# Optimization experiments

Measured on AMD Instinct MI355X. Metric: run time of the kernel, lower is better.

Reference implementation:

```python
import jax, jax.numpy as jnp
import numpy as np

N = 40000          # nodes
E = 1280000        # edges (avg degree 32)
S = 64             # num_scalars
V = 16             # num_vectors
R = 32             # num_radial
CUTOFF = 10.0


def setup_inputs() -> dict:
    key = jax.random.key(0)
    ks = jax.random.split(key, 12)
    scalars = jax.random.normal(ks[0], (N, S), dtype=jnp.float32)
    vectors = jax.random.normal(ks[1], (N, V, 3), dtype=jnp.float32)
    edge_index = jax.random.randint(ks[2], (2, E), 0, N, dtype=jnp.int64)
    edge_vec = jax.random.normal(ks[3], (E, 3), dtype=jnp.float32)
    # radial_net: Linear(R,R) -> SiLU -> Linear(R, S + 2V)
    W1 = jax.random.normal(ks[4], (R, R), dtype=jnp.float32) * 0.1
    b1 = jnp.zeros((R,), dtype=jnp.float32)
    W2 = jax.random.normal(ks[5], (R, S + 2 * V), dtype=jnp.float32) * 0.1
    b2 = jnp.zeros((S + 2 * V,), dtype=jnp.float32)
    # attention: Linear(2S+R, S) -> SiLU -> Linear(S, 1)
    Wa1 = jax.random.normal(ks[6], (2 * S + R, S), dtype=jnp.float32) * 0.1
    ba1 = jnp.zeros((S,), dtype=jnp.float32)
    Wa2 = jax.random.normal(ks[7], (S, 1), dtype=jnp.float32) * 0.1
    ba2 = jnp.zeros((1,), dtype=jnp.float32)
    return dict(scalars=scalars, vectors=vectors, edge_vec=edge_vec,
                W1=W1, b1=b1, W2=W2, b2=b2,
                Wa1=Wa1, ba1=ba1, Wa2=Wa2, ba2=ba2,
                edge_index=edge_index)


def reference(scalars, vectors, edge_vec, W1, b1, W2, b2, Wa1, ba1, Wa2, ba2, edge_index):
    src = edge_index[0]  # j (source)
    dst = edge_index[1]  # i (target / aggregation index)

    d = jnp.linalg.norm(edge_vec, axis=-1)                 # [E]
    d_safe = jnp.clip(d[:, None], 1e-8, None)              # [E,1]

    # Bessel radial basis with cosine cutoff
    freqs = (jnp.arange(1, R + 1, dtype=jnp.float32) * np.pi / CUTOFF)
    bessel = jnp.sin(freqs * d[:, None]) / d_safe          # [E,R]
    cut = 0.5 * (jnp.cos(np.pi * d[:, None] / CUTOFF) + 1.0)
    cut = cut * (d[:, None] < CUTOFF).astype(jnp.float32)
    rbf = bessel * cut                                     # [E,R]

    # spherical harmonics (lmax=1); vector already normalized, sh = [1, y, z, x]
    unit = edge_vec / d_safe                               # [E,3]
    sh_weight = jnp.stack([unit[:, 1], unit[:, 2], unit[:, 0]], axis=-1)  # [E,3]

    # radial filter MLP
    filters = jax.nn.silu(rbf @ W1 + b1) @ W2 + b2         # [E, S+2V]
    scalar_filter = filters[:, :S]
    vector_filter = filters[:, S:S + V]
    vector_gate = filters[:, S + V:]

    s_i = scalars[dst]                                     # [E,S]
    s_j = scalars[src]                                     # [E,S]
    v_j = vectors[src]                                     # [E,V,3]

    scalar_message = s_j * scalar_filter                   # [E,S]
    vector_message = (v_j * vector_filter[:, :, None]
                      + vector_gate[:, :, None] * sh_weight[:, None, :])  # [E,V,3]

    att_in = jnp.concatenate([s_i, s_j, rbf], axis=-1)     # [E, 2S+R]
    att = jax.nn.sigmoid(jax.nn.silu(att_in @ Wa1 + ba1) @ Wa2 + ba2)  # [E,1]

    scalar_message = att * scalar_message
    vector_message = att[:, :, None] * vector_message

    scalar_aggr = jax.ops.segment_sum(scalar_message, dst, num_segments=N)
    vector_aggr = jax.ops.segment_sum(vector_message, dst, num_segments=N)

    return scalars + scalar_aggr, vectors + vector_aggr
```

## Files before the change

kernel.cpp:

```cpp
#include <hip/hip_runtime.h>

static constexpr int N_ = 40000;
static constexpr int E_ = 1280000;
static constexpr int NS = N_ * 64;
static constexpr int NV = N_ * 48;

typedef _Float16 half2_t __attribute__((ext_vector_type(2)));
typedef _Float16 half8_t __attribute__((ext_vector_type(8)));
typedef float float4_t __attribute__((ext_vector_type(4)));
typedef unsigned int uint;

__device__ __forceinline__ float silu_f(float x) { return __fdividef(x, 1.f + __expf(-x)); }
__device__ __forceinline__ int rfl(int x) { return __builtin_amdgcn_readfirstlane(x); }

static constexpr int PATT_BLOCKS = 512;
__global__ __launch_bounds__(256) void k_patt(
    const float* __restrict__ scalars, const float* __restrict__ Wa1,
    const float* __restrict__ ba1,
    _Float16* __restrict__ P1h, _Float16* __restrict__ P2h)
{
    int gw   = (blockIdx.x * 256 + threadIdx.x) >> 6;
    int lane = threadIdx.x & 63;
    float w[128];
#pragma unroll
    for (int k = 0; k < 128; k++) w[k] = Wa1[k * 64 + lane];
    float bias = ba1[lane];
    for (int n = gw; n < N_; n += PATT_BLOCKS * 4) {
        float sv = scalars[(size_t)n * 64 + lane];
        float a1 = bias, a2 = 0.f;
#pragma unroll
        for (int k = 0; k < 64; k++) {
            float sk = __shfl(sv, k, 64);
            a1 = fmaf(sk, w[k], a1);
            a2 = fmaf(sk, w[64 + k], a2);
        }
        P1h[(size_t)n * 64 + lane] = (_Float16)a1;
        P2h[(size_t)n * 64 + lane] = (_Float16)a2;
    }
}

__global__ void k_convp(const float* __restrict__ scalars, const float* __restrict__ vectors,
                        _Float16* __restrict__ sc16p, _Float16* __restrict__ vec16p,
                        const float* __restrict__ W1, const float* __restrict__ Wa1,
                        const float* __restrict__ W2, uint* __restrict__ tbl,
                        uint* __restrict__ tbl2)
{
    if (blockIdx.x >= 5000) {
        int t = (blockIdx.x - 5000) * 256 + threadIdx.x;
        if (t < 1536) {
            int j = t >> 4, q = t & 15;
            int k0 = 2 * q, k1 = 2 * q + 1;
            float a = (j < 64) ? Wa1[(128 + k0) * 64 + j] : W1[k0 * 32 + (j - 64)];
            float b = (j < 64) ? Wa1[(128 + k1) * 64 + j] : W1[k1 * 32 + (j - 64)];
            half2_t v; v.x = (_Float16)a; v.y = (_Float16)b;
            tbl[t] = __builtin_bit_cast(uint, v);
        } else if (t < 3072) {
            int tt = t - 1536;
            int j = tt >> 4, q = tt & 15;
            half2_t v;
            v.x = (_Float16)W2[(2 * q + 0) * 96 + j];
            v.y = (_Float16)W2[(2 * q + 1) * 96 + j];
            tbl2[tt] = __builtin_bit_cast(uint, v);
        }
        return;
    }
    int t = blockIdx.x * 256 + threadIdx.x;
    if (t < N_ * 16) {
        int n = t >> 4, bl = t & 15;
        const float* srow = scalars + (size_t)n * 64;
        half2_t a, b;
        a.x = (_Float16)srow[bl];
        a.y = (_Float16)srow[16 + bl];
        b.x = (_Float16)srow[32 + bl];
        b.y = (_Float16)srow[48 + bl];
        uint2 u; u.x = __builtin_bit_cast(uint, a); u.y = __builtin_bit_cast(uint, b);
        *(uint2*)(sc16p + (size_t)n * 64 + bl * 4) = u;
    } else {
        int tt = t - N_ * 16;
        int n = tt >> 4, bl = tt & 15;
        const float* vrow = vectors + (size_t)n * 48 + bl * 3;
        half2_t a, b;
        a.x = (_Float16)vrow[0];
        a.y = (_Float16)vrow[1];
        b.x = (_Float16)vrow[2];
        b.y = (_Float16)0.f;
        uint2 u; u.x = __builtin_bit_cast(uint, a); u.y = __builtin_bit_cast(uint, b);
        *(uint2*)(vec16p + (size_t)n * 64 + bl * 4) = u;
    }
}

__global__ void k_rank(const int* __restrict__ eidx, int* __restrict__ cnt,
                       int* __restrict__ r)
{
    int e = blockIdx.x * 256 + threadIdx.x;
    r[e] = atomicAdd(&cnt[eidx[E_ + e]], 1);
}

__global__ void k_scan1(const int* __restrict__ cnt, int* __restrict__ row_start,
                        int* __restrict__ bsum)
{
    __shared__ int buf[1024];
    int b = blockIdx.x, tid = threadIdx.x;
    int idx = b * 1024 + tid;
    int v = (idx < N_) ? cnt[idx] : 0;
    buf[tid] = v;
    __syncthreads();
    for (int off = 1; off < 1024; off <<= 1) {
        int t = (tid >= off) ? buf[tid - off] : 0;
        __syncthreads();
        buf[tid] += t;
        __syncthreads();
    }
    if (idx < N_) row_start[idx] = buf[tid] - v;
    if (tid == 1023) bsum[b] = buf[1023];
}

__global__ void k_scan3(const int* __restrict__ bsum, int* __restrict__ row_start)
{
    __shared__ int boffs;
    if (threadIdx.x == 0) {
        int s = 0;
        for (int b = 0; b < (int)blockIdx.x; b++) s += bsum[b];
        boffs = s;
    }
    __syncthreads();
    int idx = blockIdx.x * 1024 + threadIdx.x;
    if (idx < N_) row_start[idx] += boffs;
    if (idx == N_) row_start[N_] = E_;
}

__global__ void k_place3(const int* __restrict__ eidx, const float* __restrict__ edge_vec,
                         const int* __restrict__ row_start, const int* __restrict__ r,
                         float4* __restrict__ rec)
{
    int e = blockIdx.x * 256 + threadIdx.x;
    int src = eidx[e];
    int dst = eidx[E_ + e];
    size_t slot = (size_t)(row_start[dst] + r[e]);
    uint sd = (uint)src | ((uint)dst << 16);
    rec[slot] = make_float4(edge_vec[3 * e + 0], edge_vec[3 * e + 1],
                            edge_vec[3 * e + 2], __uint_as_float(sd));
}

__global__ __launch_bounds__(256, 3) void k_edges_sorted(
    const float4* __restrict__ rec,
    const _Float16* __restrict__ P1h, const _Float16* __restrict__ P2h,
    const uint* __restrict__ tbl, const float* __restrict__ b1,
    const float* __restrict__ Wa2, const float* __restrict__ ba2,
    float4* __restrict__ attsh, int* __restrict__ srcbuf, uint* __restrict__ hbufp)
{
    __shared__ char lds_raw[4 * 8448];
    int tid = threadIdx.x;
    int wid = tid >> 6, lane = tid & 63;
    char* wbase = lds_raw + wid * 8448;
    int bl = lane & 15, bq = lane >> 4;

    int i = blockIdx.x * 256 + tid;
    float4 ra = rec[(size_t)i];
    float ev0 = ra.x, ev1 = ra.y, ev2 = ra.z;
    uint sd = __float_as_uint(ra.w);
    int src = (int)(sd & 0xffffu);
    int dst = (int)(sd >> 16);

    float d = sqrtf(fmaf(ev0, ev0, fmaf(ev1, ev1, ev2 * ev2)));
    float inv_d = __fdividef(1.f, fmaxf(d, 1e-8f));
    float cut = (d < 10.f) ? 0.5f * (__cosf(0.31415927f * d) + 1.f) : 0.f;
    float cutd = cut * inv_d;
    float sh0 = ev1 * inv_d, sh1 = ev2 * inv_d, sh2 = ev0 * inv_d;

    float th = 0.31415927f * d;
    float scur = __sinf(th);
    float twoC = 2.f * __cosf(th);
    float sprev = 0.f;
    uint rbf2[16];
#pragma unroll
    for (int q = 0; q < 16; q++) {
        float r0 = scur * cutd;
        float snext = fmaf(twoC, scur, -sprev);
        sprev = scur; scur = snext;
        float r1 = scur * cutd;
        snext = fmaf(twoC, scur, -sprev);
        sprev = scur; scur = snext;
        half2_t v; v.x = (_Float16)r0; v.y = (_Float16)r1;
        rbf2[q] = __builtin_bit_cast(uint, v);
    }
    {
        uint4* rw = (uint4*)(wbase + lane * 64);
        rw[0] = make_uint4(rbf2[0], rbf2[1], rbf2[2], rbf2[3]);
        rw[1] = make_uint4(rbf2[4], rbf2[5], rbf2[6], rbf2[7]);
        rw[2] = make_uint4(rbf2[8], rbf2[9], rbf2[10], rbf2[11]);
        rw[3] = make_uint4(rbf2[12], rbf2[13], rbf2[14], rbf2[15]);
    }
    uint4 bfr[6];
#pragma unroll
    for (int u = 0; u < 6; u++)
        bfr[u] = *(const uint4*)(tbl + (u * 16 + bl) * 16 + bq * 4);

    uint4 afr[4];
#pragma unroll
    for (int t = 0; t < 4; t++)
        afr[t] = *(const uint4*)(wbase + (t * 16 + bl) * 64 + bq * 16);

    _Float16* gtile = (_Float16*)wbase;

#pragma unroll
    for (int t = 0; t < 4; t++) {
        half8_t av = __builtin_bit_cast(half8_t, afr[t]);
        int eb = t * 16 + bq * 4;
#pragma unroll
        for (int u = 4; u < 6; u++) {
            float4_t dd = __builtin_amdgcn_mfma_f32_16x16x32_f16(
                av, __builtin_bit_cast(half8_t, bfr[u]), (float4_t)(0.f), 0, 0, 0);
            int col = (u - 4) * 16 + bl;
            gtile[(eb + 0) * 34 + col] = (_Float16)dd[0];
            gtile[(eb + 1) * 34 + col] = (_Float16)dd[1];
            gtile[(eb + 2) * 34 + col] = (_Float16)dd[2];
            gtile[(eb + 3) * 34 + col] = (_Float16)dd[3];
        }
    }
    {
        const uint* growB = (const uint*)(wbase + (size_t)lane * 68);
        uint hp[16];
#pragma unroll
        for (int q = 0; q < 16; q++) {
            half2_t gg = __builtin_bit_cast(half2_t, growB[q]);
            half2_t v;
            v.x = (_Float16)silu_f((float)gg.x + b1[2 * q + 0]);
            v.y = (_Float16)silu_f((float)gg.y + b1[2 * q + 1]);
            hp[q] = __builtin_bit_cast(uint, v);
        }
        uint4* hrow4 = (uint4*)(hbufp + (size_t)i * 16);
#pragma unroll
        for (int q = 0; q < 4; q++)
            hrow4[q] = make_uint4(hp[4 * q + 0], hp[4 * q + 1], hp[4 * q + 2], hp[4 * q + 3]);
    }

#pragma unroll
    for (int t = 0; t < 4; t++) {
        half8_t av = __builtin_bit_cast(half8_t, afr[t]);
        int eb = t * 16 + bq * 4;
#pragma unroll
        for (int u = 0; u < 4; u++) {
            float4_t dd = __builtin_amdgcn_mfma_f32_16x16x32_f16(
                av, __builtin_bit_cast(half8_t, bfr[u]), (float4_t)(0.f), 0, 0, 0);
            int col = u * 16 + bl;
            gtile[(eb + 0) * 66 + col] = (_Float16)dd[0];
            gtile[(eb + 1) * 66 + col] = (_Float16)dd[1];
            gtile[(eb + 2) * 66 + col] = (_Float16)dd[2];
            gtile[(eb + 3) * 66 + col] = (_Float16)dd[3];
        }
    }
    const uint* grow = (const uint*)(wbase + (size_t)lane * 132);

    const uint2* p1h = (const uint2*)(P1h + (size_t)dst * 64);
    const uint2* p2h = (const uint2*)(P2h + (size_t)src * 64);
    float logit = ba2[0];
#pragma unroll
    for (int q = 0; q < 16; q++) {
        uint2 ua = p1h[q];
        uint2 ub = p2h[q];
        half2_t s01 = __builtin_bit_cast(half2_t, ua.x) + __builtin_bit_cast(half2_t, ub.x)
                    + __builtin_bit_cast(half2_t, grow[2 * q + 0]);
        half2_t s23 = __builtin_bit_cast(half2_t, ua.y) + __builtin_bit_cast(half2_t, ub.y)
                    + __builtin_bit_cast(half2_t, grow[2 * q + 1]);
        logit = fmaf(silu_f((float)s01.x), Wa2[4 * q + 0], logit);
        logit = fmaf(silu_f((float)s01.y), Wa2[4 * q + 1], logit);
        logit = fmaf(silu_f((float)s23.x), Wa2[4 * q + 2], logit);
        logit = fmaf(silu_f((float)s23.y), Wa2[4 * q + 3], logit);
    }
    float att = __fdividef(1.f, 1.f + __expf(-logit));

    attsh[i] = make_float4(att, sh0, sh1, sh2);
    srcbuf[i] = src;
}

static constexpr int NPW = 5;
__global__ __launch_bounds__(256, 4) void k_gather_mfma(
    const float* __restrict__ scalars, const float* __restrict__ vectors,
    const _Float16* __restrict__ sc16p, const _Float16* __restrict__ vec16p,
    const float* __restrict__ b2,
    const int* __restrict__ row_start,
    const float4* __restrict__ attsh, const int* __restrict__ srcbuf,
    const uint* __restrict__ hbuf, const uint* __restrict__ tbl2,
    float* __restrict__ out)
{
    int wid  = threadIdx.x >> 6;
    int lane = threadIdx.x & 63;
    int gw   = blockIdx.x * 4 + wid;
    int bl = lane & 15, bq = lane >> 4;

    uint4 bfr2[6];
#pragma unroll
    for (int u = 0; u < 6; u++)
        bfr2[u] = *(const uint4*)(tbl2 + (u * 16 + bl) * 16 + bq * 4);

    float b2s[4];
#pragma unroll
    for (int u = 0; u < 4; u++) b2s[u] = b2[u * 16 + bl];
    float bvf = b2[64 + bl], bvg = b2[80 + bl];

    int n0 = gw * NPW;
    for (int nn = 0; nn < NPW; nn++) {
        int n = n0 + nn;
        int rs = rfl(row_start[n]);
        int re = rfl(row_start[n + 1]);

        float accS0 = 0.f, accS1 = 0.f, accS2 = 0.f, accS3 = 0.f;
        float accV0 = 0.f, accV1 = 0.f, accV2 = 0.f;

        for (int i0 = rs; i0 < re; i0 += 16) {
            uint4 av4 = make_uint4(0u, 0u, 0u, 0u);
            if (i0 + bl < re)
                av4 = *(const uint4*)(hbuf + (size_t)(i0 + bl) * 16 + bq * 4);
            half8_t av = __builtin_bit_cast(half8_t, av4);

            float4_t d0 = __builtin_amdgcn_mfma_f32_16x16x32_f16(av, __builtin_bit_cast(half8_t, bfr2[0]), (float4_t)(0.f), 0, 0, 0);
            float4_t d1 = __builtin_amdgcn_mfma_f32_16x16x32_f16(av, __builtin_bit_cast(half8_t, bfr2[1]), (float4_t)(0.f), 0, 0, 0);
            float4_t d2 = __builtin_amdgcn_mfma_f32_16x16x32_f16(av, __builtin_bit_cast(half8_t, bfr2[2]), (float4_t)(0.f), 0, 0, 0);
            float4_t d3 = __builtin_amdgcn_mfma_f32_16x16x32_f16(av, __builtin_bit_cast(half8_t, bfr2[3]), (float4_t)(0.f), 0, 0, 0);
            float4_t d4 = __builtin_amdgcn_mfma_f32_16x16x32_f16(av, __builtin_bit_cast(half8_t, bfr2[4]), (float4_t)(0.f), 0, 0, 0);
            float4_t d5 = __builtin_amdgcn_mfma_f32_16x16x32_f16(av, __builtin_bit_cast(half8_t, bfr2[5]), (float4_t)(0.f), 0, 0, 0);

#pragma unroll
            for (int r = 0; r < 4; r++) {
                int slot = i0 + bq * 4 + r;
                int ok = (slot < re);
                int cs = ok ? slot : (re - 1);
                float4 as = attsh[cs];
                float att = ok ? as.x : 0.f;
                int src = srcbuf[cs];
                uint2 su = *(const uint2*)(sc16p + (size_t)src * 64 + bl * 4);
                uint2 vu = *(const uint2*)(vec16p + (size_t)src * 64 + bl * 4);
                half2_t s01 = __builtin_bit_cast(half2_t, su.x);
                half2_t s23 = __builtin_bit_cast(half2_t, su.y);
                half2_t v01 = __builtin_bit_cast(half2_t, vu.x);
                half2_t v23 = __builtin_bit_cast(half2_t, vu.y);
                accS0 = fmaf(att * (float)s01.x, d0[r] + b2s[0], accS0);
                accS1 = fmaf(att * (float)s01.y, d1[r] + b2s[1], accS1);
                accS2 = fmaf(att * (float)s23.x, d2[r] + b2s[2], accS2);
                accS3 = fmaf(att * (float)s23.y, d3[r] + b2s[3], accS3);
                float vf = d4[r] + bvf;
                float vg = d5[r] + bvg;
                accV0 = fmaf(att, fmaf((float)v01.x, vf, vg * as.y), accV0);
                accV1 = fmaf(att, fmaf((float)v01.y, vf, vg * as.z), accV1);
                accV2 = fmaf(att, fmaf((float)v23.x, vf, vg * as.w), accV2);
            }
        }

        accS0 += __shfl_xor(accS0, 16, 64); accS0 += __shfl_xor(accS0, 32, 64);
        accS1 += __shfl_xor(accS1, 16, 64); accS1 += __shfl_xor(accS1, 32, 64);
        accS2 += __shfl_xor(accS2, 16, 64); accS2 += __shfl_xor(accS2, 32, 64);
        accS3 += __shfl_xor(accS3, 16, 64); accS3 += __shfl_xor(accS3, 32, 64);
        accV0 += __shfl_xor(accV0, 16, 64); accV0 += __shfl_xor(accV0, 32, 64);
        accV1 += __shfl_xor(accV1, 16, 64); accV1 += __shfl_xor(accV1, 32, 64);
        accV2 += __shfl_xor(accV2, 16, 64); accV2 += __shfl_xor(accV2, 32, 64);

        if (bq == 0) {
            size_t o = (size_t)n * 64 + bl;
            out[o +  0] = scalars[o +  0] + accS0;
            out[o + 16] = scalars[o + 16] + accS1;
            out[o + 32] = scalars[o + 32] + accS2;
            out[o + 48] = scalars[o + 48] + accS3;
            size_t ov = (size_t)n * 48 + 3 * bl;
            out[NS + ov + 0] = vectors[ov + 0] + accV0;
            out[NS + ov + 1] = vectors[ov + 1] + accV1;
            out[NS + ov + 2] = vectors[ov + 2] + accV2;
        }
    }
}

extern "C" void kernel_launch(void* const* d_in, const int* in_sizes, int n_in,
                              void* d_out, int out_size, void* d_ws, size_t ws_size,
                              hipStream_t stream)
{
    const float* scalars  = (const float*)d_in[0];
    const float* vectors  = (const float*)d_in[1];
    const float* edge_vec = (const float*)d_in[2];
    const float* W1  = (const float*)d_in[3];
    const float* b1  = (const float*)d_in[4];
    const float* W2  = (const float*)d_in[5];
    const float* b2  = (const float*)d_in[6];
    const float* Wa1 = (const float*)d_in[7];
    const float* ba1 = (const float*)d_in[8];
    const float* Wa2 = (const float*)d_in[9];
    const float* ba2 = (const float*)d_in[10];
    const int* eidx  = (const int*)d_in[11];

    char* wsb = (char*)d_ws;
    float4* attsh = (float4*)wsb;
    float*  P1    = (float*)(wsb + (size_t)E_ * 16);
    float*  P2    = P1 + NS;
    float*  hbuf  = P2 + NS;
    int* cnt       = (int*)(hbuf + (size_t)32 * E_);
    int* bsum      = cnt + N_;
    int* row_start = cnt + 2 * N_;
    int* perm      = row_start + N_ + 1;
    int* srcbuf    = perm + E_;
    int*  rnk  = (int*)hbuf;
    uint* tbl  = (uint*)hbuf + (size_t)16 * E_;
    uint* tbl2 = tbl + 1536;
    _Float16* P1h  = (_Float16*)(tbl2 + 1536);
    _Float16* P2h  = P1h + NS;
    _Float16* sc16p = P2h + NS;
    _Float16* vec16p = (_Float16*)P1;
    float4* rec = (float4*)(sc16p + NS);

    hipMemsetAsync(cnt, 0, (size_t)N_ * sizeof(int), stream);
    k_rank<<<5000, 256, 0, stream>>>(eidx, cnt, rnk);
    k_scan1<<<40, 1024, 0, stream>>>(cnt, row_start, bsum);
    k_scan3<<<40, 1024, 0, stream>>>(bsum, row_start);
    k_place3<<<5000, 256, 0, stream>>>(eidx, edge_vec, row_start, rnk, rec);
    k_patt<<<PATT_BLOCKS, 256, 0, stream>>>(scalars, Wa1, ba1, P1h, P2h);
    k_convp<<<5012, 256, 0, stream>>>(scalars, vectors, sc16p, vec16p, W1, Wa1, W2, tbl, tbl2);
    k_edges_sorted<<<5000, 256, 0, stream>>>(rec, P1h, P2h,
                                             tbl, b1, Wa2, ba2,
                                             attsh, srcbuf, (uint*)hbuf);
    k_gather_mfma<<<2000, 256, 0, stream>>>(scalars, vectors, sc16p, vec16p, b2, row_start,
                                            attsh, srcbuf, (const uint*)hbuf, tbl2,
                                            (float*)d_out);
}
```

Before: 357.8 us.

## Replace global atomic counting sort with per-block LDS histograms

Replaces the global-atomic destination counting (k_rank plus memset) with 40 blocks that each build a full 40000-bin histogram in shared memory over a contiguous edge chunk. A column-wise scan over the per-block counts then produces per-block offsets, and the placement kernel combines row_start, the block offset and the local rank. The aim is to avoid contended global atomics, at the cost of only 40 blocks occupying the GPU during histogramming, about 160KB of LDS per block, and extra cntB traffic in the scan and placement.

```diff
diff --git a/kernel.cpp b/kernel.cpp
--- a/kernel.cpp
+++ b/kernel.cpp
@@ -4,6 +4,8 @@
 static constexpr int E_ = 1280000;
 static constexpr int NS = N_ * 64;
 static constexpr int NV = N_ * 48;
+static constexpr int HB = 40;
+static constexpr int CHUNK = E_ / HB;
 
 typedef _Float16 half2_t __attribute__((ext_vector_type(2)));
 typedef _Float16 half8_t __attribute__((ext_vector_type(8)));
@@ -12,6 +14,74 @@
 
 __device__ __forceinline__ float silu_f(float x) { return __fdividef(x, 1.f + __expf(-x)); }
 __device__ __forceinline__ int rfl(int x) { return __builtin_amdgcn_readfirstlane(x); }
+
+__global__ __launch_bounds__(1024) void k_hist(
+    const int* __restrict__ eidx, int* __restrict__ cntB, int* __restrict__ rloc)
+{
+    __shared__ int bins[N_];
+    int b = blockIdx.x, tid = threadIdx.x;
+    for (int j = tid; j < N_; j += 1024) bins[j] = 0;
+    __syncthreads();
+    int e0 = b * CHUNK;
+    for (int e = e0 + tid; e < e0 + CHUNK; e += 1024)
+        rloc[e] = atomicAdd(&bins[eidx[E_ + e]], 1);
+    __syncthreads();
+    for (int j = tid; j < N_; j += 1024) cntB[b * N_ + j] = bins[j];
+}
+
+__global__ void k_scanB(int* __restrict__ cntB, int* __restrict__ row_start,
+                        int* __restrict__ bsum)
+{
+    __shared__ int buf[1024];
+    int b = blockIdx.x, tid = threadIdx.x;
+    int idx = b * 1024 + tid;
+    int v = 0;
+    if (idx < N_) {
+        for (int c = 0; c < HB; c++) {
+            int t = cntB[c * N_ + idx];
+            cntB[c * N_ + idx] = v;
+            v += t;
+        }
+    }
+    buf[tid] = v;
+    __syncthreads();
+    for (int off = 1; off < 1024; off <<= 1) {
+        int t = (tid >= off) ? buf[tid - off] : 0;
+        __syncthreads();
+        buf[tid] += t;
+        __syncthreads();
+    }
+    if (idx < N_) row_start[idx] = buf[tid] - v;
+    if (tid == 1023) bsum[b] = buf[1023];
+}
+
+__global__ void k_scan3(const int* __restrict__ bsum, int* __restrict__ row_start)
+{
+    __shared__ int boffs;
+    if (threadIdx.x == 0) {
+        int s = 0;
+        for (int b = 0; b < (int)blockIdx.x; b++) s += bsum[b];
+        boffs = s;
+    }
+    __syncthreads();
+    int idx = blockIdx.x * 1024 + threadIdx.x;
+    if (idx < N_) row_start[idx] += boffs;
+    if (idx == N_) row_start[N_] = E_;
+}
+
+__global__ void k_place3b(const int* __restrict__ eidx, const float* __restrict__ edge_vec,
+                          const int* __restrict__ row_start, const int* __restrict__ cntB,
+                          const int* __restrict__ rloc, float4* __restrict__ rec)
+{
+    int e = blockIdx.x * 256 + threadIdx.x;
+    int src = eidx[e];
+    int dst = eidx[E_ + e];
+    int b = e / CHUNK;
+    size_t slot = (size_t)(row_start[dst] + cntB[b * N_ + dst] + rloc[e]);
+    uint sd = (uint)src | ((uint)dst << 16);
+    rec[slot] = make_float4(edge_vec[3 * e + 0], edge_vec[3 * e + 1],
+                            edge_vec[3 * e + 2], __uint_as_float(sd));
+}
 
 static constexpr int PATT_BLOCKS = 512;
 __global__ __launch_bounds__(256) void k_patt(
@@ -87,59 +157,6 @@
         uint2 u; u.x = __builtin_bit_cast(uint, a); u.y = __builtin_bit_cast(uint, b);
         *(uint2*)(vec16p + (size_t)n * 64 + bl * 4) = u;
     }
-}
-
-__global__ void k_rank(const int* __restrict__ eidx, int* __restrict__ cnt,
-                       int* __restrict__ r)
-{
-    int e = blockIdx.x * 256 + threadIdx.x;
-    r[e] = atomicAdd(&cnt[eidx[E_ + e]], 1);
-}
-
-__global__ void k_scan1(const int* __restrict__ cnt, int* __restrict__ row_start,
-                        int* __restrict__ bsum)
-{
-    __shared__ int buf[1024];
-    int b = blockIdx.x, tid = threadIdx.x;
-    int idx = b * 1024 + tid;
-    int v = (idx < N_) ? cnt[idx] : 0;
-    buf[tid] = v;
-    __syncthreads();
-    for (int off = 1; off < 1024; off <<= 1) {
-        int t = (tid >= off) ? buf[tid - off] : 0;
-        __syncthreads();
-        buf[tid] += t;
-        __syncthreads();
-    }
-    if (idx < N_) row_start[idx] = buf[tid] - v;
-    if (tid == 1023) bsum[b] = buf[1023];
-}
-
-__global__ void k_scan3(const int* __restrict__ bsum, int* __restrict__ row_start)
-{
-    __shared__ int boffs;
-    if (threadIdx.x == 0) {
-        int s = 0;
-        for (int b = 0; b < (int)blockIdx.x; b++) s += bsum[b];
-        boffs = s;
-    }
-    __syncthreads();
-    int idx = blockIdx.x * 1024 + threadIdx.x;
-    if (idx < N_) row_start[idx] += boffs;
-    if (idx == N_) row_start[N_] = E_;
-}
-
-__global__ void k_place3(const int* __restrict__ eidx, const float* __restrict__ edge_vec,
-                         const int* __restrict__ row_start, const int* __restrict__ r,
-                         float4* __restrict__ rec)
-{
-    int e = blockIdx.x * 256 + threadIdx.x;
-    int src = eidx[e];
-    int dst = eidx[E_ + e];
-    size_t slot = (size_t)(row_start[dst] + r[e]);
-    uint sd = (uint)src | ((uint)dst << 16);
-    rec[slot] = make_float4(edge_vec[3 * e + 0], edge_vec[3 * e + 1],
-                            edge_vec[3 * e + 2], __uint_as_float(sd));
 }
 
 __global__ __launch_bounds__(256, 3) void k_edges_sorted(
@@ -396,7 +413,7 @@
     int* row_start = cnt + 2 * N_;
     int* perm      = row_start + N_ + 1;
     int* srcbuf    = perm + E_;
-    int*  rnk  = (int*)hbuf;
+    int*  rloc = (int*)hbuf;
     uint* tbl  = (uint*)hbuf + (size_t)16 * E_;
     uint* tbl2 = tbl + 1536;
     _Float16* P1h  = (_Float16*)(tbl2 + 1536);
@@ -404,12 +421,12 @@
     _Float16* sc16p = P2h + NS;
     _Float16* vec16p = (_Float16*)P1;
     float4* rec = (float4*)(sc16p + NS);
-
-    hipMemsetAsync(cnt, 0, (size_t)N_ * sizeof(int), stream);
-    k_rank<<<5000, 256, 0, stream>>>(eidx, cnt, rnk);
-    k_scan1<<<40, 1024, 0, stream>>>(cnt, row_start, bsum);
+    int* cntB   = (int*)(rec + E_);
+
+    k_hist<<<HB, 1024, 0, stream>>>(eidx, cntB, rloc);
+    k_scanB<<<40, 1024, 0, stream>>>(cntB, row_start, bsum);
     k_scan3<<<40, 1024, 0, stream>>>(bsum, row_start);
-    k_place3<<<5000, 256, 0, stream>>>(eidx, edge_vec, row_start, rnk, rec);
+    k_place3b<<<5000, 256, 0, stream>>>(eidx, edge_vec, row_start, cntB, rloc, rec);
     k_patt<<<PATT_BLOCKS, 256, 0, stream>>>(scalars, Wa1, ba1, P1h, P2h);
     k_convp<<<5012, 256, 0, stream>>>(scalars, vectors, sc16p, vec16p, W1, Wa1, W2, tbl, tbl2);
     k_edges_sorted<<<5000, 256, 0, stream>>>(rec, P1h, P2h,
```

Measured after the change: 353.4 us. Within noise of the previous version (-1.2%).
